# Kernel tuning notes

Measured on AMD Instinct MI355X. Metric: run time of the kernel, lower is better.

Reference implementation:

```python
import jax, jax.numpy as jnp
import numpy as np

KH, KW, STRIDE, PAD = 3, 3, 2, 1


def _unfold(x, kh, kw, stride, pad):
    # torch.nn.Unfold: [B,C,H,W] -> [B, C*kh*kw, L], channel-major ordering (c, i, j)
    x = jnp.pad(x, ((0, 0), (0, 0), (pad, pad), (pad, pad)))
    B, C, H, W = x.shape
    oh = (H - kh) // stride + 1
    ow = (W - kw) // stride + 1
    patches = jnp.stack(
        [x[:, :, i:i + stride * (oh - 1) + 1:stride, j:j + stride * (ow - 1) + 1:stride]
         for i in range(kh) for j in range(kw)],
        axis=2,
    )  # [B, C, kh*kw, oh, ow]
    return patches.reshape(B, C * kh * kw, oh * ow)


def _fold(w, out_size, kh, kw, stride, pad):
    # torch.nn.functional.fold: [B, C*kh*kw, L] -> [B, C, H, W], sum of overlaps
    B = w.shape[0]
    C = w.shape[1] // (kh * kw)
    H, W = out_size
    oh = (H + 2 * pad - kh) // stride + 1
    ow = (W + 2 * pad - kw) // stride + 1
    w = w.reshape(B, C, kh, kw, oh, ow)
    out = jnp.zeros((B, C, H + 2 * pad, W + 2 * pad), dtype=w.dtype)
    for i in range(kh):
        for j in range(kw):
            out = out.at[:, :, i:i + stride * (oh - 1) + 1:stride,
                         j:j + stride * (ow - 1) + 1:stride].add(w[:, :, i, j])
    return out[:, :, pad:pad + H, pad:pad + W]


def setup_inputs() -> dict:
    key = jax.random.key(0)
    k1, k2, k3, k4 = jax.random.split(key, 4)
    C = 256
    feat = jax.random.normal(k1, (4, C, 64, 64), jnp.float32)
    src = jax.random.normal(k2, (4, C, 128, 128), jnp.float32)
    scale = 1.0 / np.sqrt(C)
    Wq = jax.random.normal(k3, (C, C), jnp.float32) * scale
    Wv = jax.random.normal(k4, (C, C), jnp.float32) * scale
    bq = jnp.zeros((C,), jnp.float32)
    bv = jnp.zeros((C,), jnp.float32)
    return {"feat": feat, "src": src, "Wq": Wq, "bq": bq, "Wv": Wv, "bv": bv}


def reference(feat, src, Wq, bq, Wv, bv):
    B, C, H, W = src.shape
    # q head: conv1x1(src) then 3x3/stride2/pad1 unfold -> [B, C, 9, L]
    qc = jnp.einsum('oi,bihw->bohw', Wq, src) + bq[None, :, None, None]
    q = _unfold(qc, KH, KW, STRIDE, PAD).reshape(B, C, KH * KW, -1)
    # v head: conv1x1(feat) flattened -> [B, C, D]; k head: feat flattened
    vc = jnp.einsum('oi,bihw->bohw', Wv, feat) + bv[None, :, None, None]
    v = vc.reshape(B, C, -1)
    k = feat.reshape(B, C, -1)
    # per-channel attention over the 9 window positions
    scale = jnp.asarray(1.0 / np.sqrt(q.shape[-1]), q.dtype)
    A = jax.nn.softmax(jnp.einsum('bckd,bcd->bck', q, k) * scale, axis=-1)  # [B,C,9]
    weights = jnp.einsum('bck,bcd->bckd', A, v).reshape(B, C * KH * KW, -1)
    return _fold(weights, (H, W), KH, KW, STRIDE, PAD) * src
```

## Files before the change

kernel.cpp:

```cpp
#include <hip/hip_runtime.h>

typedef _Float16 f16;
typedef _Float16 f16x2 __attribute__((ext_vector_type(2)));
typedef _Float16 f16x4 __attribute__((ext_vector_type(4)));
typedef _Float16 f16x8 __attribute__((ext_vector_type(8)));
typedef float f32x4 __attribute__((ext_vector_type(4)));

#define BB 4
#define CC 256
#define HH 128
#define WW 128
#define OWW 64
#define DD 4096
#define NPIX 16384
#define CP 264

__global__ __launch_bounds__(256) void prep_all_k(const float* __restrict__ Wq,
                                                  const float* __restrict__ Wv,
                                                  const float* __restrict__ src,
                                                  const float* __restrict__ feat,
                                                  f16* __restrict__ wqh,
                                                  f16* __restrict__ wvh,
                                                  f16* __restrict__ wvl,
                                                  f16* __restrict__ srcT,
                                                  f16* __restrict__ fth,
                                                  f16* __restrict__ ftl) {
    __shared__ float L[64][129];
    int bigid = blockIdx.x;
    int t = threadIdx.x;
    if (bigid < 16) {
        int bb = bigid;
        bool isQ = (bb < 8);
        const float* W = isQ ? Wq : Wv;
        int tt = (bb & 7) * 256 + t;
        int G = tt >> 8, o = tt & 255;
#pragma unroll
        for (int kk = 0; kk < 4; ++kk) {
            const float* wr = W + (size_t)o * CC + kk * 64 + G * 8;
            float4 a = *(const float4*)wr;
            float4 b2 = *(const float4*)(wr + 4);
            float v[8] = {a.x, a.y, a.z, a.w, b2.x, b2.y, b2.z, b2.w};
            f16x8 hv, lv;
#pragma unroll
            for (int e = 0; e < 8; ++e) {
                f16 hh = (f16)v[e];
                hv[e] = hh;
                lv[e] = (f16)(v[e] - (float)hh);
            }
            size_t idx = (size_t)(((kk * 8 + G) * 256) + o) * 8;
            if (isQ) {
                *(f16x8*)&wqh[idx] = hv;
            } else {
                *(f16x8*)&wvh[idx] = hv;
                *(f16x8*)&wvl[idx] = lv;
            }
        }
    } else if (bigid < 16 + 2048) {
        int bid = bigid - 16;
        int pxt = bid & 127, ct = (bid >> 7) & 3, b = bid >> 9;
        int c0 = ct * 64, px0 = pxt * 128;
        const float* S = src + ((size_t)b * CC + c0) * NPIX + px0;
#pragma unroll
        for (int i = 0; i < 8; ++i) {
            int idx = i * 256 + t;
            int cl = idx >> 5, p4 = (idx & 31) * 4;
            *(float4*)&L[cl][p4] = *(const float4*)(S + (size_t)cl * NPIX + p4);
        }
        __syncthreads();
        f16* D = srcT + ((size_t)b * NPIX + px0) * CP + c0;
#pragma unroll
        for (int i = 0; i < 4; ++i) {
            int idx = i * 256 + t;
            int pl = idx >> 3, cg = (idx & 7) * 8;
            f16x8 v;
#pragma unroll
            for (int e = 0; e < 8; ++e) v[e] = (f16)L[cg + e][pl];
            *(f16x8*)&D[(size_t)pl * CP + cg] = v;
        }
    } else {
        int bid = bigid - 16 - 2048;
        int dt = bid & 31, ct = (bid >> 5) & 3, b = bid >> 7;
        int c0 = ct * 64, d0 = dt * 128;
        const float* S = feat + ((size_t)b * CC + c0) * DD + d0;
#pragma unroll
        for (int i = 0; i < 8; ++i) {
            int idx = i * 256 + t;
            int cl = idx >> 5, p4 = (idx & 31) * 4;
            *(float4*)&L[cl][p4] = *(const float4*)(S + (size_t)cl * DD + p4);
        }
        __syncthreads();
        size_t base = ((size_t)b * DD + d0) * CP + c0;
#pragma unroll
        for (int i = 0; i < 4; ++i) {
            int idx = i * 256 + t;
            int dl = idx >> 3, cg = (idx & 7) * 8;
            f16x8 hv, lv;
#pragma unroll
            for (int e = 0; e < 8; ++e) {
                float x = L[cg + e][dl];
                f16 hh = (f16)x;
                hv[e] = hh;
                lv[e] = (f16)(x - (float)hh);
            }
            *(f16x8*)&fth[base + (size_t)dl * CP + cg] = hv;
            *(f16x8*)&ftl[base + (size_t)dl * CP + cg] = lv;
        }
    }
}

__global__ __launch_bounds__(512, 4) void qv_k(const f16* __restrict__ srcT,
                                               const float* __restrict__ feat,
                                               const f16* __restrict__ wqh,
                                               const float* __restrict__ bq,
                                               float* __restrict__ dotp,
                                               const f16* __restrict__ fth,
                                               const f16* __restrict__ ftl,
                                               const f16* __restrict__ wvh,
                                               const f16* __restrict__ wvl,
                                               const float* __restrict__ bv,
                                               f16* __restrict__ vh) {
    int t = threadIdx.x;
    if (blockIdx.x < 512) {
        __shared__ __align__(16) f16 Fl[512 * 36];
        int bid = blockIdx.x;
        int b = bid >> 7;
        int hp = (bid >> 1) & 63;
        int wh = bid & 1;
        int h = hp * 2;
        int w0 = wh * 64;
        int x0 = wh * 32;
        int ybase = hp;

        {
            const float* fb = feat + (size_t)b * CC * DD;
            int o = t >> 1, yi = t & 1;
            int y = ybase + yi;
            const float* frow = fb + (size_t)o * DD + y * 64 + x0;
            f16* dst = &Fl[(o * 2 + yi) * 36];
            if (y < 64) {
#pragma unroll
                for (int k2 = 0; k2 < 8; ++k2) {
                    float4 f = *(const float4*)&frow[k2 * 4];
                    f16x4 hv = {(f16)f.x, (f16)f.y, (f16)f.z, (f16)f.w};
                    *(f16x4*)&dst[k2 * 4] = hv;
                }
                dst[32] = (x0 + 32 < 64) ? (f16)frow[32] : (f16)0.f;
            } else {
                f16x4 z = {0, 0, 0, 0};
#pragma unroll
                for (int k2 = 0; k2 < 8; ++k2) *(f16x4*)&dst[k2 * 4] = z;
                dst[32] = (f16)0.f;
            }
        }
        __syncthreads();

        int wv = t >> 6;
        int lane = t & 63;
        int g = lane >> 4;
        int col = lane & 15;
        int rh = wv >> 2;
        int o0 = (wv & 3) * 64;

        f32x4 acc[4][4];
#pragma unroll
        for (int mf = 0; mf < 4; ++mf)
#pragma unroll
            for (int nf = 0; nf < 4; ++nf) acc[mf][nf] = (f32x4){0.f, 0.f, 0.f, 0.f};

        const f16* sTw = srcT + ((size_t)b * NPIX + (size_t)(h + rh) * WW + w0) * CP;

#pragma unroll
        for (int kk = 0; kk < 4; ++kk) {
#pragma unroll
            for (int s = 0; s < 2; ++s) {
                int G = s * 4 + g;
                int cb = kk * 64 + G * 8;
                f16x8 af[4], bh[4];
#pragma unroll
                for (int mf = 0; mf < 4; ++mf)
                    af[mf] = *(const f16x8*)&sTw[(size_t)(mf * 16 + col) * CP + cb];
#pragma unroll
                for (int nf = 0; nf < 4; ++nf) {
                    size_t idx = (size_t)(((kk * 8 + G) * 256) + o0 + nf * 16 + col) * 8;
                    bh[nf] = *(const f16x8*)&wqh[idx];
                }
#pragma unroll
                for (int mf = 0; mf < 4; ++mf)
#pragma unroll
                    for (int nf = 0; nf < 4; ++nf)
                        acc[mf][nf] = __builtin_amdgcn_mfma_f32_16x16x32_f16(af[mf], bh[nf], acc[mf][nf], 0, 0, 0);
            }
        }

        int i0 = rh ? 2 : 1;
        float bqv[4];
#pragma unroll
        for (int nf = 0; nf < 4; ++nf) bqv[nf] = bq[o0 + nf * 16 + col];

        float bins[4][2][3];
#pragma unroll
        for (int nf = 0; nf < 4; ++nf)
#pragma unroll
            for (int ii = 0; ii < 2; ++ii)
#pragma unroll
                for (int j = 0; j < 3; ++j) bins[nf][ii][j] = 0.f;

#pragma unroll
        for (int mf = 0; mf < 4; ++mf) {
            int X = mf * 8 + g * 2;
#pragma unroll
            for (int ii = 0; ii < 2; ++ii) {
                if (ii == 1 && rh == 0) continue;
#pragma unroll
                for (int nf = 0; nf < 4; ++nf) {
                    int o = o0 + nf * 16 + col;
                    const f16* fr = &Fl[(o * 2 + ii) * 36];
                    f16x2 lh = *(const f16x2*)&fr[X];
                    float lo = (float)lh[0], hi = (float)lh[1];
                    float s2 = (float)fr[X + 2];
                    float qv0 = acc[mf][nf][0] + bqv[nf];
                    float qv1 = acc[mf][nf][1] + bqv[nf];
                    float qv2 = acc[mf][nf][2] + bqv[nf];
                    float qv3 = acc[mf][nf][3] + bqv[nf];
                    bins[nf][ii][1] += qv0 * lo + qv2 * hi;
                    bins[nf][ii][2] += qv1 * lo + qv3 * hi;
                    bins[nf][ii][0] += qv1 * hi + qv3 * s2;
                }
            }
        }

#pragma unroll
        for (int m = 16; m <= 32; m <<= 1)
#pragma unroll
            for (int nf = 0; nf < 4; ++nf)
#pragma unroll
                for (int ii = 0; ii < 2; ++ii) {
                    if (ii == 1 && rh == 0) continue;
#pragma unroll
                    for (int j = 0; j < 3; ++j)
                        bins[nf][ii][j] += __shfl_xor(bins[nf][ii][j], m, 64);
                }

        if (g == 0) {
            float* dslot = dotp + (size_t)(bid & 127) * (9 * BB * CC);
#pragma unroll
            for (int nf = 0; nf < 4; ++nf) {
                int bc = b * CC + o0 + nf * 16 + col;
                dslot[(i0 * 3 + 0) * (BB * CC) + bc] = bins[nf][0][0];
                dslot[(i0 * 3 + 1) * (BB * CC) + bc] = bins[nf][0][1];
                dslot[(i0 * 3 + 2) * (BB * CC) + bc] = bins[nf][0][2];
                if (rh) {
                    dslot[0 * (BB * CC) + bc] = bins[nf][1][0];
                    dslot[1 * (BB * CC) + bc] = bins[nf][1][1];
                    dslot[2 * (BB * CC) + bc] = bins[nf][1][2];
                }
            }
        }
    } else {
        int bid = blockIdx.x - 512;
        int b = bid >> 6;
        int rest = bid & 63;
        int ot = rest >> 4;
        int dt = rest & 15;

        int wv = t >> 6;
        int wm = wv >> 2;
        int wn = wv & 3;
        int lane = t & 63;
        int g = lane >> 4;
        int col = lane & 15;

        int o_w = ot * 64 + wm * 32;
        int d_w = dt * 256 + wn * 64;

        f32x4 acc[2][4];
#pragma unroll
        for (int mf = 0; mf < 2; ++mf)
#pragma unroll
            for (int nf = 0; nf < 4; ++nf) acc[mf][nf] = (f32x4){0.f, 0.f, 0.f, 0.f};

        const f16* fthb = fth + (size_t)b * DD * CP;
        const f16* ftlb = ftl + (size_t)b * DD * CP;

#pragma unroll
        for (int kk = 0; kk < 4; ++kk) {
#pragma unroll
            for (int s = 0; s < 2; ++s) {
                int G = s * 4 + g;
                int cb = kk * 64 + G * 8;
                f16x8 bh[4], bl[4], ah[2], al[2];
#pragma unroll
                for (int nf = 0; nf < 4; ++nf) {
                    size_t off = (size_t)(d_w + nf * 16 + col) * CP + cb;
                    bh[nf] = *(const f16x8*)&fthb[off];
                    bl[nf] = *(const f16x8*)&ftlb[off];
                }
#pragma unroll
                for (int mf = 0; mf < 2; ++mf) {
                    size_t idx = (size_t)(((kk * 8 + G) * 256) + o_w + mf * 16 + col) * 8;
                    ah[mf] = *(const f16x8*)&wvh[idx];
                    al[mf] = *(const f16x8*)&wvl[idx];
                }
#pragma unroll
                for (int mf = 0; mf < 2; ++mf)
#pragma unroll
                    for (int nf = 0; nf < 4; ++nf)
                        acc[mf][nf] = __builtin_amdgcn_mfma_f32_16x16x32_f16(ah[mf], bh[nf], acc[mf][nf], 0, 0, 0);
#pragma unroll
                for (int mf = 0; mf < 2; ++mf)
#pragma unroll
                    for (int nf = 0; nf < 4; ++nf)
                        acc[mf][nf] = __builtin_amdgcn_mfma_f32_16x16x32_f16(al[mf], bh[nf], acc[mf][nf], 0, 0, 0);
#pragma unroll
                for (int mf = 0; mf < 2; ++mf)
#pragma unroll
                    for (int nf = 0; nf < 4; ++nf)
                        acc[mf][nf] = __builtin_amdgcn_mfma_f32_16x16x32_f16(ah[mf], bl[nf], acc[mf][nf], 0, 0, 0);
            }
        }

        f16* vb = vh + (size_t)b * CC * DD;
#pragma unroll
        for (int mf = 0; mf < 2; ++mf)
#pragma unroll
            for (int nf = 0; nf < 4; ++nf) {
#pragma unroll
                for (int r = 0; r < 4; ++r) {
                    int o = o_w + mf * 16 + g * 4 + r;
                    int d = d_w + nf * 16 + col;
                    vb[(size_t)o * DD + d] = (f16)(acc[mf][nf][r] + bv[o]);
                }
            }
    }
}

__global__ __launch_bounds__(288) void redsm_k(const float* __restrict__ dotp,
                                               float* __restrict__ A) {
    __shared__ float sl[9][33];
    int t = threadIdx.x;
    if (t < 288) {
        int k = t / 32, bcl = t % 32;
        int bc = blockIdx.x * 32 + bcl;
        float s = 0.f;
#pragma unroll 16
        for (int p = 0; p < 128; ++p)
            s += dotp[(size_t)p * (9 * BB * CC) + k * (BB * CC) + bc];
        sl[k][bcl] = s;
    }
    __syncthreads();
    if (t < 32) {
        int bc = blockIdx.x * 32 + t;
        float s[9];
        float m = -1e30f;
        const float sc = 1.f / 64.f;
#pragma unroll
        for (int k = 0; k < 9; ++k) { s[k] = sl[k][t] * sc; m = fmaxf(m, s[k]); }
        float sum = 0.f;
#pragma unroll
        for (int k = 0; k < 9; ++k) { s[k] = __expf(s[k] - m); sum += s[k]; }
        float inv = 1.f / sum;
#pragma unroll
        for (int k = 0; k < 9; ++k) A[(size_t)bc * 9 + k] = s[k] * inv;
    }
}

__global__ __launch_bounds__(256) void out_k(const float* __restrict__ src,
                                             const f16* __restrict__ vh,
                                             const float* __restrict__ A,
                                             float* __restrict__ out) {
    __shared__ float Al[9];
    int bid = blockIdx.x;
    int bc = bid >> 4;
    int h0 = (bid & 15) << 3;
    int t = threadIdx.x;
    if (t < 9) Al[t] = A[(size_t)bc * 9 + t];
    __syncthreads();
    int h = h0 + (t >> 5);
    int a = t & 31;
    bool hodd = (h & 1) != 0;
    int iA = hodd ? 2 : 1;
    int yA = hodd ? ((h - 1) >> 1) : (h >> 1);
    int yB = (h + 1) >> 1;
    bool hasB = hodd && (yB < 64);

    const f16* vb = vh + (size_t)bc * DD;
    float s0 = 0.f, s1 = 0.f, s2 = 0.f, s3 = 0.f;
    {
        const f16* vr = vb + yA * OWW + 2 * a;
        f16x2 v01 = *(const f16x2*)vr;
        float V0 = (float)v01[0], V1 = (float)v01[1];
        float V2 = (2 * a + 2 < 64) ? (float)vr[2] : 0.f;
        float A0 = Al[iA * 3 + 0], A1 = Al[iA * 3 + 1], A2 = Al[iA * 3 + 2];
        s0 += A1 * V0;
        s1 += A0 * V1 + A2 * V0;
        s2 += A1 * V1;
        s3 += A0 * V2 + A2 * V1;
    }
    if (hasB) {
        const f16* vr = vb + yB * OWW + 2 * a;
        f16x2 v01 = *(const f16x2*)vr;
        float V0 = (float)v01[0], V1 = (float)v01[1];
        float V2 = (2 * a + 2 < 64) ? (float)vr[2] : 0.f;
        float A0 = Al[0], A1 = Al[1], A2 = Al[2];
        s0 += A1 * V0;
        s1 += A0 * V1 + A2 * V0;
        s2 += A1 * V1;
        s3 += A0 * V2 + A2 * V1;
    }
    size_t idx = (size_t)bc * NPIX + (size_t)h * WW + a * 4;
    float4 sv = *(const float4*)(src + idx);
    float4 o4;
    o4.x = s0 * sv.x; o4.y = s1 * sv.y; o4.z = s2 * sv.z; o4.w = s3 * sv.w;
    *(float4*)(out + idx) = o4;
}

extern "C" void kernel_launch(void* const* d_in, const int* in_sizes, int n_in,
                              void* d_out, int out_size, void* d_ws, size_t ws_size,
                              hipStream_t stream) {
    const float* feat = (const float*)d_in[0];
    const float* src  = (const float*)d_in[1];
    const float* Wq   = (const float*)d_in[2];
    const float* bq   = (const float*)d_in[3];
    const float* Wv   = (const float*)d_in[4];
    const float* bv   = (const float*)d_in[5];
    float* out = (float*)d_out;

    f16*   vh   = (f16*)d_ws;
    float* dotp = (float*)(vh + (size_t)BB * CC * DD);
    float* A    = dotp + (size_t)128 * 9 * BB * CC;
    f16*   wqh  = (f16*)(A + (size_t)BB * CC * 9);
    f16*   wvh  = wqh + 65536;
    f16*   wvl  = wvh + 65536;
    f16*   srcT = wvl + 65536;
    f16*   fth  = srcT + (size_t)BB * NPIX * CP;
    f16*   ftl  = fth + (size_t)BB * DD * CP;

    prep_all_k<<<16 + 2048 + 512, 256, 0, stream>>>(Wq, Wv, src, feat,
                                                    wqh, wvh, wvl, srcT, fth, ftl);
    qv_k<<<768, 512, 0, stream>>>(srcT, feat, wqh, bq, dotp,
                                  fth, ftl, wvh, wvl, bv, vh);
    redsm_k<<<BB * CC / 32, 288, 0, stream>>>(dotp, A);
    out_k<<<BB * CC * 16, 256, 0, stream>>>(src, vh, A, out);
}
```

Measured before the change: 104.3 us.

## Double qv_k block size to 1024 threads, splitting pixel work across more waves

The fused q/v kernel now runs 1024-thread blocks. In the q branch each wave handles half the pixel columns (32 instead of 64), and the two halves' partial bins are combined through shared memory before being written to dotp. The v branch covers twice the d-range per block, so the grid drops from 768 to 640 blocks. The aim is fewer accumulator registers per wave and more waves in flight. The cost is an extra barrier, extra shared-memory traffic, and possible register or occupancy pressure with launch_bounds(1024,4).

After: 111.6 us. +7.0%, slower.

```diff
diff --git a/kernel.cpp b/kernel.cpp
--- a/kernel.cpp
+++ b/kernel.cpp
@@ -108,20 +108,21 @@
     }
 }
 
-__global__ __launch_bounds__(512, 4) void qv_k(const f16* __restrict__ srcT,
-                                               const float* __restrict__ feat,
-                                               const f16* __restrict__ wqh,
-                                               const float* __restrict__ bq,
-                                               float* __restrict__ dotp,
-                                               const f16* __restrict__ fth,
-                                               const f16* __restrict__ ftl,
-                                               const f16* __restrict__ wvh,
-                                               const f16* __restrict__ wvl,
-                                               const float* __restrict__ bv,
-                                               f16* __restrict__ vh) {
+__global__ __launch_bounds__(1024, 4) void qv_k(const f16* __restrict__ srcT,
+                                                const float* __restrict__ feat,
+                                                const f16* __restrict__ wqh,
+                                                const float* __restrict__ bq,
+                                                float* __restrict__ dotp,
+                                                const f16* __restrict__ fth,
+                                                const f16* __restrict__ ftl,
+                                                const f16* __restrict__ wvh,
+                                                const f16* __restrict__ wvl,
+                                                const float* __restrict__ bv,
+                                                f16* __restrict__ vh) {
     int t = threadIdx.x;
     if (blockIdx.x < 512) {
         __shared__ __align__(16) f16 Fl[512 * 36];
+        __shared__ float binsh[8][4][16][6];
         int bid = blockIdx.x;
         int b = bid >> 7;
         int hp = (bid >> 1) & 63;
@@ -133,23 +134,24 @@
 
         {
             const float* fb = feat + (size_t)b * CC * DD;
-            int o = t >> 1, yi = t & 1;
+            int o = t >> 2, sub = t & 3;
+            int yi = sub >> 1, xh = sub & 1;
             int y = ybase + yi;
-            const float* frow = fb + (size_t)o * DD + y * 64 + x0;
-            f16* dst = &Fl[(o * 2 + yi) * 36];
+            const float* frow = fb + (size_t)o * DD + y * 64 + x0 + xh * 16;
+            f16* dst = &Fl[(o * 2 + yi) * 36 + xh * 16];
             if (y < 64) {
 #pragma unroll
-                for (int k2 = 0; k2 < 8; ++k2) {
+                for (int k2 = 0; k2 < 4; ++k2) {
                     float4 f = *(const float4*)&frow[k2 * 4];
                     f16x4 hv = {(f16)f.x, (f16)f.y, (f16)f.z, (f16)f.w};
                     *(f16x4*)&dst[k2 * 4] = hv;
                 }
-                dst[32] = (x0 + 32 < 64) ? (f16)frow[32] : (f16)0.f;
+                if (xh == 1) dst[16] = (x0 + 32 < 64) ? (f16)frow[16] : (f16)0.f;
             } else {
                 f16x4 z = {0, 0, 0, 0};
 #pragma unroll
-                for (int k2 = 0; k2 < 8; ++k2) *(f16x4*)&dst[k2 * 4] = z;
-                dst[32] = (f16)0.f;
+                for (int k2 = 0; k2 < 4; ++k2) *(f16x4*)&dst[k2 * 4] = z;
+                if (xh == 1) dst[16] = (f16)0.f;
             }
         }
         __syncthreads();
@@ -158,16 +160,18 @@
         int lane = t & 63;
         int g = lane >> 4;
         int col = lane & 15;
-        int rh = wv >> 2;
-        int o0 = (wv & 3) * 64;
-
-        f32x4 acc[4][4];
-#pragma unroll
-        for (int mf = 0; mf < 4; ++mf)
+        int pxh = wv & 1;
+        int o0 = ((wv >> 1) & 3) * 64;
+        int rh = wv >> 3;
+        int widx = rh * 4 + ((wv >> 1) & 3);
+
+        f32x4 acc[2][4];
+#pragma unroll
+        for (int mf = 0; mf < 2; ++mf)
 #pragma unroll
             for (int nf = 0; nf < 4; ++nf) acc[mf][nf] = (f32x4){0.f, 0.f, 0.f, 0.f};
 
-        const f16* sTw = srcT + ((size_t)b * NPIX + (size_t)(h + rh) * WW + w0) * CP;
+        const f16* sTw = srcT + ((size_t)b * NPIX + (size_t)(h + rh) * WW + w0 + pxh * 32) * CP;
 
 #pragma unroll
         for (int kk = 0; kk < 4; ++kk) {
@@ -175,9 +179,9 @@
             for (int s = 0; s < 2; ++s) {
                 int G = s * 4 + g;
                 int cb = kk * 64 + G * 8;
-                f16x8 af[4], bh[4];
-#pragma unroll
-                for (int mf = 0; mf < 4; ++mf)
+                f16x8 af[2], bh[4];
+#pragma unroll
+                for (int mf = 0; mf < 2; ++mf)
                     af[mf] = *(const f16x8*)&sTw[(size_t)(mf * 16 + col) * CP + cb];
 #pragma unroll
                 for (int nf = 0; nf < 4; ++nf) {
@@ -185,7 +189,7 @@
                     bh[nf] = *(const f16x8*)&wqh[idx];
                 }
 #pragma unroll
-                for (int mf = 0; mf < 4; ++mf)
+                for (int mf = 0; mf < 2; ++mf)
 #pragma unroll
                     for (int nf = 0; nf < 4; ++nf)
                         acc[mf][nf] = __builtin_amdgcn_mfma_f32_16x16x32_f16(af[mf], bh[nf], acc[mf][nf], 0, 0, 0);
@@ -206,8 +210,8 @@
                 for (int j = 0; j < 3; ++j) bins[nf][ii][j] = 0.f;
 
 #pragma unroll
-        for (int mf = 0; mf < 4; ++mf) {
-            int X = mf * 8 + g * 2;
+        for (int mf = 0; mf < 2; ++mf) {
+            int X = pxh * 16 + mf * 8 + g * 2;
 #pragma unroll
             for (int ii = 0; ii < 2; ++ii) {
                 if (ii == 1 && rh == 0) continue;
@@ -241,37 +245,50 @@
                         bins[nf][ii][j] += __shfl_xor(bins[nf][ii][j], m, 64);
                 }
 
-        if (g == 0) {
+        if (pxh == 1 && g == 0) {
+#pragma unroll
+            for (int nf = 0; nf < 4; ++nf)
+#pragma unroll
+                for (int ii = 0; ii < 2; ++ii)
+#pragma unroll
+                    for (int j = 0; j < 3; ++j)
+                        binsh[widx][nf][col][ii * 3 + j] = bins[nf][ii][j];
+        }
+        __syncthreads();
+        if (pxh == 0 && g == 0) {
             float* dslot = dotp + (size_t)(bid & 127) * (9 * BB * CC);
 #pragma unroll
             for (int nf = 0; nf < 4; ++nf) {
                 int bc = b * CC + o0 + nf * 16 + col;
-                dslot[(i0 * 3 + 0) * (BB * CC) + bc] = bins[nf][0][0];
-                dslot[(i0 * 3 + 1) * (BB * CC) + bc] = bins[nf][0][1];
-                dslot[(i0 * 3 + 2) * (BB * CC) + bc] = bins[nf][0][2];
+                float b00 = bins[nf][0][0] + binsh[widx][nf][col][0];
+                float b01 = bins[nf][0][1] + binsh[widx][nf][col][1];
+                float b02 = bins[nf][0][2] + binsh[widx][nf][col][2];
+                dslot[(i0 * 3 + 0) * (BB * CC) + bc] = b00;
+                dslot[(i0 * 3 + 1) * (BB * CC) + bc] = b01;
+                dslot[(i0 * 3 + 2) * (BB * CC) + bc] = b02;
                 if (rh) {
-                    dslot[0 * (BB * CC) + bc] = bins[nf][1][0];
-                    dslot[1 * (BB * CC) + bc] = bins[nf][1][1];
-                    dslot[2 * (BB * CC) + bc] = bins[nf][1][2];
+                    dslot[0 * (BB * CC) + bc] = bins[nf][1][0] + binsh[widx][nf][col][3];
+                    dslot[1 * (BB * CC) + bc] = bins[nf][1][1] + binsh[widx][nf][col][4];
+                    dslot[2 * (BB * CC) + bc] = bins[nf][1][2] + binsh[widx][nf][col][5];
                 }
             }
         }
     } else {
         int bid = blockIdx.x - 512;
-        int b = bid >> 6;
-        int rest = bid & 63;
-        int ot = rest >> 4;
-        int dt = rest & 15;
+        int b = bid >> 5;
+        int rest = bid & 31;
+        int ot = rest >> 3;
+        int dt = rest & 7;
 
         int wv = t >> 6;
-        int wm = wv >> 2;
-        int wn = wv & 3;
+        int wm = wv >> 3;
+        int wn = wv & 7;
         int lane = t & 63;
         int g = lane >> 4;
         int col = lane & 15;
 
         int o_w = ot * 64 + wm * 32;
-        int d_w = dt * 256 + wn * 64;
+        int d_w = dt * 512 + wn * 64;
 
         f32x4 acc[2][4];
 #pragma unroll
@@ -437,8 +454,8 @@
 
     prep_all_k<<<16 + 2048 + 512, 256, 0, stream>>>(Wq, Wv, src, feat,
                                                     wqh, wvh, wvl, srcT, fth, ftl);
-    qv_k<<<768, 512, 0, stream>>>(srcT, feat, wqh, bq, dotp,
-                                  fth, ftl, wvh, wvl, bv, vh);
+    qv_k<<<512 + 128, 1024, 0, stream>>>(srcT, feat, wqh, bq, dotp,
+                                         fth, ftl, wvh, wvl, bv, vh);
     redsm_k<<<BB * CC / 32, 288, 0, stream>>>(dotp, A);
     out_k<<<BB * CC * 16, 256, 0, stream>>>(src, vh, A, out);
 }
```
